# Kernel tuning notes

Hardware: AMD Instinct MI355X
Metric: run time of the kernel (lower is better)

Reference implementation:

```python
import jax, jax.numpy as jnp
import numpy as np
import math

D = 1024
H = 16
HD = D // H

def layernorm(x, g, b, eps=1e-5):
    mu = jnp.mean(x, axis=-1, keepdims=True)
    var = jnp.var(x, axis=-1, keepdims=True)
    return (x - mu) * jax.lax.rsqrt(var + eps) * g + b

def setup_inputs() -> dict:
    key = jax.random.key(0)
    ks = jax.random.split(key, 12)
    s = 0.02
    return {
        "x": jax.random.normal(ks[0], (2, 2048, D), jnp.float32),
        "Wk": jax.random.normal(ks[1], (D, D), jnp.float32) * s,
        "Wq": jax.random.normal(ks[2], (D, D), jnp.float32) * s,
        "Wv": jax.random.normal(ks[3], (D, D), jnp.float32) * s,
        "Wp": jax.random.normal(ks[4], (D, D), jnp.float32) * s,
        "bp": jnp.zeros((D,), jnp.float32),
        "g1": jnp.ones((D,), jnp.float32),
        "b1": jnp.zeros((D,), jnp.float32),
        "g2": jnp.ones((D,), jnp.float32),
        "b2": jnp.zeros((D,), jnp.float32),
        "W1": jax.random.normal(ks[5], (D, 4 * D), jnp.float32) * s,
        "bm1": jnp.zeros((4 * D,), jnp.float32),
        "W2": jax.random.normal(ks[6], (4 * D, D), jnp.float32) * s,
        "bm2": jnp.zeros((D,), jnp.float32),
    }

def reference(x, Wk, Wq, Wv, Wp, bp, g1, b1, g2, b2, W1, bm1, W2, bm2):
    B, S, _ = x.shape
    xn = layernorm(x, g1, b1)  # pre-LN; residual uses xn (faithful to source)
    # project and split heads -> [B, H, S, HD]
    def heads(y):
        return y.reshape(B, S, H, HD).transpose(0, 2, 1, 3)
    q = heads(xn @ Wq)
    k = heads(xn @ Wk)
    v = heads(xn @ Wv)
    scale = 1.0 / math.sqrt(HD)
    att = jnp.einsum('bhsd,bhtd->bhst', q, k) * scale  # [B,H,S,S]
    diag = jnp.eye(S, dtype=bool)
    att = jnp.where(diag, -jnp.inf, att)  # exclude self-attention on diagonal
    att = jax.nn.softmax(att, axis=-1)
    y = jnp.einsum('bhst,bhtd->bhsd', att, v)
    y = y.transpose(0, 2, 1, 3).reshape(B, S, D)
    y = y @ Wp + bp  # dropout is identity at inference
    h = xn + y
    hn = layernorm(h, g2, b2)
    mlp = jax.nn.gelu(hn @ W1 + bm1, approximate=False) @ W2 + bm2
    return h + mlp
```

## Files before the change

kernel.cpp:

```cpp
#include <hip/hip_runtime.h>
#include <hip/hip_bf16.h>
#include <math.h>

#define BATCH   2
#define SEQ     2048
#define D_MODEL 1024
#define NHEAD   16
#define HEADD   64
#define NROWS   (BATCH * SEQ)
#define D_FF    4096
#define TPARTS  4
#define TSPAN   (SEQ / TPARTS)

typedef __bf16 bf16_t;
typedef __bf16 bf16x2 __attribute__((ext_vector_type(2)));
typedef __bf16 bf16x4 __attribute__((ext_vector_type(4)));
typedef __bf16 bf16x8 __attribute__((ext_vector_type(8)));
typedef float  f32x4  __attribute__((ext_vector_type(4)));

#define QSCALE 0.18033688011112042f

__device__ __forceinline__ void gload_lds16(const void* g, void* l) {
    __builtin_amdgcn_global_load_lds(
        (const __attribute__((address_space(1))) unsigned int*)g,
        (__attribute__((address_space(3))) unsigned int*)l, 16, 0, 0);
}

__global__ __launch_bounds__(256) void transpose_all6(
    const float* __restrict__ Wq, const float* __restrict__ Wk,
    const float* __restrict__ Wv, const float* __restrict__ Wp,
    const float* __restrict__ W1, const float* __restrict__ W2,
    bf16_t* __restrict__ Wqkvt, bf16_t* __restrict__ Wpt,
    bf16_t* __restrict__ W1t, bf16_t* __restrict__ W2t)
{
    __shared__ float tile[32][33];
    int bid = blockIdx.x;
    const float* W; bf16_t* Wt; int K, N, n0, k0;
    if (bid < 4096) {
        int seg = bid >> 10, t = bid & 1023;
        W  = (seg == 0) ? Wq : (seg == 1) ? Wk : (seg == 2) ? Wv : Wp;
        Wt = (seg < 3) ? (Wqkvt + (size_t)seg * 1024 * 1024) : Wpt;
        K = 1024; N = 1024;
        n0 = (t & 31) * 32; k0 = (t >> 5) * 32;
    } else if (bid < 8192) {
        int t = bid - 4096;
        W = W1; Wt = W1t; K = 1024; N = 4096;
        n0 = (t & 127) * 32; k0 = (t >> 7) * 32;
    } else {
        int t = bid - 8192;
        W = W2; Wt = W2t; K = 4096; N = 1024;
        n0 = (t & 31) * 32; k0 = (t >> 5) * 32;
    }
    int tx = threadIdx.x;
    int ty = threadIdx.y;
    #pragma unroll
    for (int i = 0; i < 32; i += 8)
        tile[ty + i][tx] = W[(size_t)(k0 + ty + i) * N + n0 + tx];
    __syncthreads();
    #pragma unroll
    for (int i = 0; i < 32; i += 8)
        Wt[(size_t)(n0 + ty + i) * K + k0 + tx] = (bf16_t)tile[tx][ty + i];
}

__global__ __launch_bounds__(256) void ln_kernel(
    const float* __restrict__ x, const float* __restrict__ g,
    const float* __restrict__ b, bf16_t* __restrict__ out)
{
    int row = blockIdx.x;
    int tid = threadIdx.x;
    const float* xr = x + (size_t)row * D_MODEL;
    f32x4 v = *(const f32x4*)(xr + tid * 4);
    float s  = v[0] + v[1] + v[2] + v[3];
    float s2 = v[0]*v[0] + v[1]*v[1] + v[2]*v[2] + v[3]*v[3];
    #pragma unroll
    for (int off = 32; off; off >>= 1) {
        s  += __shfl_down(s, off);
        s2 += __shfl_down(s2, off);
    }
    __shared__ float ps[4], ps2[4];
    int w = tid >> 6, lane = tid & 63;
    if (lane == 0) { ps[w] = s; ps2[w] = s2; }
    __syncthreads();
    float sum  = ps[0] + ps[1] + ps[2] + ps[3];
    float sum2 = ps2[0] + ps2[1] + ps2[2] + ps2[3];
    float mu  = sum * (1.0f / D_MODEL);
    float var = sum2 * (1.0f / D_MODEL) - mu * mu;
    float rs  = rsqrtf(var + 1e-5f);
    #pragma unroll
    for (int j = 0; j < 4; ++j) {
        int c = tid * 4 + j;
        out[(size_t)row * D_MODEL + c] = (bf16_t)((v[j] - mu) * rs * g[c] + b[c]);
    }
}

__global__ __launch_bounds__(512) void gemm256_gelu(
    const bf16_t* __restrict__ A, const bf16_t* __restrict__ Bt,
    const float* __restrict__ bias, bf16_t* __restrict__ out,
    int M, int N, int K)
{
    __shared__ bf16_t As[2][256 * 64];
    __shared__ bf16_t Bs[2][256 * 64];
    int tid = threadIdx.x;
    int bid = blockIdx.x;
    int m0 = (bid & 15) * 256;
    int n0 = (bid >> 4) * 256;
    int w = tid >> 6, lane = tid & 63, quad = lane >> 4, l15 = lane & 15;
    int wm = (w >> 2) * 128;
    int wn = (w & 3) * 64;
    int rxs = l15 & 7;

    int srow = tid >> 3;
    int sxor = (((tid & 7) ^ (srow & 7)) << 3);
    const bf16_t* Ap = A  + (size_t)(m0 + srow) * K + sxor;
    const bf16_t* Bp = Bt + (size_t)(n0 + srow) * K + sxor;

    f32x4 acc[8][4] = {};

    int nt = K >> 6;
    {
        bf16_t* AsW = &As[0][w * 512];
        bf16_t* BsW = &Bs[0][w * 512];
        #pragma unroll
        for (int h = 0; h < 2; ++h)
            #pragma unroll
            for (int p = 0; p < 2; ++p) {
                gload_lds16(Ap + (size_t)(h * 128 + p * 64) * K, AsW + h * 8192 + p * 4096);
                gload_lds16(Bp + (size_t)(h * 128 + p * 64) * K, BsW + h * 8192 + p * 4096);
            }
    }

    for (int t = 0; t < nt; ++t) {
        int cur = t & 1;
        const bf16_t* Asc = &As[cur][0];
        const bf16_t* Bsc = &Bs[cur][0];
        bf16_t* AsN = &As[cur ^ 1][w * 512];
        bf16_t* BsN = &Bs[cur ^ 1][w * 512];
        bool pf = (t + 1 < nt);
        int k1 = (t + 1) << 6;
        asm volatile("s_waitcnt vmcnt(0)" ::: "memory");
        __builtin_amdgcn_s_barrier();
        __builtin_amdgcn_sched_barrier(0);

        bf16x8 bfr[4][2];
        #pragma unroll
        for (int q = 0; q < 4; ++q) {
            bf16x8 af[2][2];
            #pragma unroll
            for (int ii = 0; ii < 2; ++ii)
                #pragma unroll
                for (int kk = 0; kk < 2; ++kk)
                    af[ii][kk] = *(const bf16x8*)&Asc[(wm + (2 * q + ii) * 16 + l15) * 64
                                                      + (((kk * 4 + quad) ^ rxs) << 3)];
            if (q == 0) {
                #pragma unroll
                for (int j = 0; j < 4; ++j)
                    #pragma unroll
                    for (int kk = 0; kk < 2; ++kk)
                        bfr[j][kk] = *(const bf16x8*)&Bsc[(wn + j * 16 + l15) * 64
                                                          + (((kk * 4 + quad) ^ rxs) << 3)];
            }
            if (q == 0 && pf) {
                #pragma unroll
                for (int h = 0; h < 2; ++h)
                    #pragma unroll
                    for (int p = 0; p < 2; ++p)
                        gload_lds16(Ap + (size_t)(h * 128 + p * 64) * K + k1,
                                    AsN + h * 8192 + p * 4096);
            }
            if (q == 1 && pf) {
                #pragma unroll
                for (int h = 0; h < 2; ++h)
                    #pragma unroll
                    for (int p = 0; p < 2; ++p)
                        gload_lds16(Bp + (size_t)(h * 128 + p * 64) * K + k1,
                                    BsN + h * 8192 + p * 4096);
            }
            __builtin_amdgcn_s_barrier();
            asm volatile("s_waitcnt lgkmcnt(0)" ::: "memory");
            __builtin_amdgcn_sched_barrier(0);
            __builtin_amdgcn_s_setprio(1);
            #pragma unroll
            for (int ii = 0; ii < 2; ++ii)
                #pragma unroll
                for (int j = 0; j < 4; ++j)
                    #pragma unroll
                    for (int kk = 0; kk < 2; ++kk)
                        acc[2 * q + ii][j] = __builtin_amdgcn_mfma_f32_16x16x32_bf16(
                            af[ii][kk], bfr[j][kk], acc[2 * q + ii][j], 0, 0, 0);
            __builtin_amdgcn_s_setprio(0);
            __builtin_amdgcn_sched_barrier(0);
            __builtin_amdgcn_s_barrier();
        }
    }

    #pragma unroll
    for (int i = 0; i < 8; ++i)
    #pragma unroll
    for (int j = 0; j < 4; ++j) {
        int col  = n0 + wn + j * 16 + l15;
        int row0 = m0 + wm + i * 16 + quad * 4;
        float bv = bias[col];
        #pragma unroll
        for (int r = 0; r < 4; ++r) {
            int row = row0 + r;
            float u = acc[i][j][r] + bv;
            float y = u * (0.7978845608028654f + 0.03567740814f * u * u);
            float e = __builtin_amdgcn_exp2f(2.8853900817779268f * y);
            float r8 = __builtin_amdgcn_rcpf(e + 1.0f);
            out[(size_t)row * N + col] = (bf16_t)(u - u * r8);
        }
    }
}

template<int EPI, int BN>
__global__ __launch_bounds__(256) void gemm128(
    const bf16_t* __restrict__ A, const bf16_t* __restrict__ Bt,
    const float* __restrict__ bias, const void* __restrict__ resid,
    void* __restrict__ out, int M, int N, int K, int RY)
{
    constexpr int JN = BN / 32;
    constexpr int NBUF = (BN == 64) ? 3 : 2;
    __shared__ bf16_t As[NBUF][128 * 64];
    __shared__ bf16_t Bs[NBUF][BN * 64];
    int tid = threadIdx.x;
    int bid = blockIdx.x;
    int cx = bid & 3, cy = (bid >> 2) & 1, i0 = bid >> 3;
    int m0 = ((cx << 3) + (i0 & 7)) << 7;
    int n0 = (cy * RY + (i0 >> 3)) * BN;
    int w = tid >> 6, lane = tid & 63, quad = lane >> 4, l15 = lane & 15;
    int wm = (w & 1) * 64, wn = (w >> 1) * (BN / 2);
    int srow = tid >> 3;
    int sxor = (((tid & 7) ^ (srow & 7)) << 3);

    const bf16_t* Ap = A  + (size_t)(m0 + srow) * K + sxor;
    const bf16_t* Bp = Bt + (size_t)(n0 + srow) * K + sxor;

    int rxs = l15 & 7;

    auto stage = [&](int buf, int k0) {
        bf16_t* AsW = &As[buf][w * 512];
        bf16_t* BsW = &Bs[buf][w * 512];
        #pragma unroll
        for (int p = 0; p < 4; ++p)
            gload_lds16(Ap + (size_t)p * 32 * K + k0, AsW + p * 2048);
        #pragma unroll
        for (int p = 0; p < JN; ++p)
            gload_lds16(Bp + (size_t)p * 32 * K + k0, BsW + p * 2048);
    };

    f32x4 acc[4][JN] = {};

    int nt = K >> 6;
    stage(0, 0);
    if (NBUF == 3 && nt > 1) stage(1, 64);
    for (int t = 0; t < nt; ++t) {
        int cur = t % NBUF;
        if constexpr (NBUF == 3) {
            if (t + 2 < nt) {
                stage((t + 2) % NBUF, (t + 2) << 6);
                asm volatile("s_waitcnt vmcnt(12)" ::: "memory");
            } else if (t + 1 < nt) {
                asm volatile("s_waitcnt vmcnt(6)" ::: "memory");
            } else {
                asm volatile("s_waitcnt vmcnt(0)" ::: "memory");
            }
        } else {
            if (t + 1 < nt) {
                stage((t + 1) % NBUF, (t + 1) << 6);
                asm volatile("s_waitcnt vmcnt(8)" ::: "memory");
            } else {
                asm volatile("s_waitcnt vmcnt(0)" ::: "memory");
            }
        }
        __builtin_amdgcn_s_barrier();
        __builtin_amdgcn_sched_barrier(0);
        #pragma unroll
        for (int kk = 0; kk < 2; ++kk) {
            bf16x8 af[4], bfr[JN];
            #pragma unroll
            for (int i = 0; i < 4; ++i)
                af[i] = *(const bf16x8*)&As[cur][(wm + i * 16 + l15) * 64
                                            + ((((kk << 2) | quad) ^ rxs) << 3)];
            #pragma unroll
            for (int j = 0; j < JN; ++j)
                bfr[j] = *(const bf16x8*)&Bs[cur][(wn + j * 16 + l15) * 64
                                            + ((((kk << 2) | quad) ^ rxs) << 3)];
            #pragma unroll
            for (int i = 0; i < 4; ++i)
                #pragma unroll
                for (int j = 0; j < JN; ++j)
                    acc[i][j] = __builtin_amdgcn_mfma_f32_16x16x32_bf16(af[i], bfr[j], acc[i][j], 0, 0, 0);
        }
        __builtin_amdgcn_sched_barrier(0);
        asm volatile("s_waitcnt lgkmcnt(0)" ::: "memory");
        __builtin_amdgcn_s_barrier();
        __builtin_amdgcn_sched_barrier(0);
    }

    #pragma unroll
    for (int i = 0; i < 4; ++i)
    #pragma unroll
    for (int j = 0; j < JN; ++j) {
        int col  = n0 + wn + j * 16 + l15;
        int row0 = m0 + wm + i * 16 + quad * 4;
        if (EPI == 6) {
            int region = (n0 + wn + j * 16) >> 10;
            if (region < 2) {
                #pragma unroll
                for (int r = 0; r < 4; ++r) {
                    int row = row0 + r;
                    float v = acc[i][j][r];
                    if (region == 0) v *= QSCALE;
                    int b = row >> 11, s = row & 2047, hh = (col & 1023) >> 6, d = col & 63;
                    bf16_t* dst = (bf16_t*)out + (size_t)region * 4194304;
                    dst[(((size_t)(b * NHEAD + hh)) * SEQ + s) * HEADD + d] = (bf16_t)v;
                }
            } else {
                int dg = col - 2048, hh = dg >> 6, d = dg & 63;
                int b = row0 >> 11, s0 = row0 & 2047;
                bf16x4 pv;
                #pragma unroll
                for (int r = 0; r < 4; ++r) pv[r] = (bf16_t)acc[i][j][r];
                *(bf16x4*)((bf16_t*)out + 8388608
                           + (((size_t)(b * NHEAD + hh)) * HEADD + d) * SEQ + s0) = pv;
            }
        } else {
            float bv = bias[col];
            #pragma unroll
            for (int r = 0; r < 4; ++r) {
                int row = row0 + r;
                float vacc = acc[i][j][r] + bv;
                if (EPI == 1) {
                    float res = (float)((const bf16_t*)resid)[(size_t)row * N + col];
                    ((float*)out)[(size_t)row * N + col] = vacc + res;
                } else {
                    float res = ((const float*)resid)[(size_t)row * N + col];
                    ((float*)out)[(size_t)row * N + col] = vacc + res;
                }
            }
        }
    }
}

__global__ __launch_bounds__(256, 4) void attn_kernel(
    const bf16_t* __restrict__ q, const bf16_t* __restrict__ k,
    const bf16_t* __restrict__ vt, bf16_t* __restrict__ po,
    float* __restrict__ plsum)
{
    int gid = blockIdx.x;
    int xcd = gid & 7;
    int loc = gid >> 3;
    int bh  = xcd * 4 + (loc >> 6);
    int rest = loc & 63;
    int qt   = rest >> 2;
    int part = rest & 3;
    int tb0 = part * TSPAN, tend = tb0 + TSPAN;
    int b = bh >> 4, h = bh & 15;
    int tid = threadIdx.x, w = tid >> 6, lane = tid & 63;
    int quad = lane >> 4, l15 = lane & 15;
    int qbase = qt * 128 + w * 32;
    const bf16_t* qh = q  + (size_t)bh * SEQ * HEADD;
    const bf16_t* kh = k  + (size_t)bh * SEQ * HEADD;
    const bf16_t* vh = vt + (size_t)bh * HEADD * SEQ;

    bf16x8 qa[2][2];
    #pragma unroll
    for (int m = 0; m < 2; ++m)
        #pragma unroll
        for (int hf = 0; hf < 2; ++hf)
            qa[m][hf] = *(const bf16x8*)(qh + (size_t)(qbase + m * 16 + l15) * HEADD + hf * 32 + quad * 8);

    bf16x8 ones;
    #pragma unroll
    for (int j = 0; j < 8; ++j) ones[j] = (bf16_t)1.0f;

    __shared__ alignas(16) bf16_t Ks[32 * 72];
    __shared__ alignas(16) bf16_t Vs[64 * 40];
    __shared__ alignas(16) bf16_t Pl[4][32][40];

    int ksrow = tid >> 3, kscol = (tid & 7) * 8;
    int vsrow = tid >> 2, vscol = (tid & 3) * 8;
    const bf16_t* kg = kh + (size_t)ksrow * HEADD + kscol;
    const bf16_t* vg = vh + (size_t)vsrow * SEQ + vscol;

    f32x4 o[2][4] = {};
    f32x4 ls[2] = {};

    for (int t0 = tb0; t0 < tend; t0 += 32) {
        bf16x8 kreg = *(const bf16x8*)(kg + (size_t)t0 * HEADD);
        bf16x8 vreg = *(const bf16x8*)(vg + t0);
        __syncthreads();
        *(bf16x8*)&Ks[ksrow * 72 + kscol] = kreg;
        *(bf16x8*)&Vs[vsrow * 40 + vscol] = vreg;
        __syncthreads();

        bf16x8 kb[2][2], vf[4];
        #pragma unroll
        for (int jt = 0; jt < 2; ++jt)
            #pragma unroll
            for (int hf = 0; hf < 2; ++hf)
                kb[jt][hf] = *(const bf16x8*)&Ks[(2 * l15 + jt) * 72 + hf * 32 + quad * 8];
        #pragma unroll
        for (int dn = 0; dn < 4; ++dn)
            vf[dn] = *(const bf16x8*)&Vs[(dn * 16 + l15) * 40 + quad * 8];

        #pragma unroll
        for (int m = 0; m < 2; ++m) {
            f32x4 sc[2];
            #pragma unroll
            for (int jt = 0; jt < 2; ++jt) {
                f32x4 z = {};
                z = __builtin_amdgcn_mfma_f32_16x16x32_bf16(qa[m][0], kb[jt][0], z, 0, 0, 0);
                z = __builtin_amdgcn_mfma_f32_16x16x32_bf16(qa[m][1], kb[jt][1], z, 0, 0, 0);
                sc[jt] = z;
            }
            int qm = qbase + m * 16;
            bool dg = (t0 < qm + 16) && (t0 + 32 > qm);
            #pragma unroll
            for (int r = 0; r < 4; ++r) {
                int qrow = qm + quad * 4 + r;
                float p0 = __builtin_amdgcn_exp2f(sc[0][r]);
                float p1 = __builtin_amdgcn_exp2f(sc[1][r]);
                if (dg) {
                    int tg = t0 + 2 * l15;
                    if (tg == qrow)     p0 = 0.0f;
                    if (tg + 1 == qrow) p1 = 0.0f;
                }
                bf16x2 pp = { (bf16_t)p0, (bf16_t)p1 };
                *(bf16x2*)&Pl[w][m * 16 + quad * 4 + r][2 * l15] = pp;
            }
        }
        #pragma unroll
        for (int m = 0; m < 2; ++m) {
            bf16x8 pf = *(const bf16x8*)&Pl[w][m * 16 + l15][quad * 8];
            ls[m] = __builtin_amdgcn_mfma_f32_16x16x32_bf16(pf, ones, ls[m], 0, 0, 0);
            #pragma unroll
            for (int dn = 0; dn < 4; ++dn)
                o[m][dn] = __builtin_amdgcn_mfma_f32_16x16x32_bf16(pf, vf[dn], o[m][dn], 0, 0, 0);
        }
    }

    #pragma unroll
    for (int m = 0; m < 2; ++m)
        #pragma unroll
        for (int dn = 0; dn < 4; ++dn)
            #pragma unroll
            for (int r = 0; r < 4; ++r) {
                int qrow = qbase + m * 16 + quad * 4 + r;
                po[(((size_t)part * NROWS) + b * SEQ + qrow) * D_MODEL
                   + h * HEADD + dn * 16 + l15] = (bf16_t)o[m][dn][r];
            }
    if (l15 == 0) {
        #pragma unroll
        for (int m = 0; m < 2; ++m)
            #pragma unroll
            for (int r = 0; r < 4; ++r) {
                int qrow = qbase + m * 16 + quad * 4 + r;
                plsum[((size_t)part * 32 + bh) * SEQ + qrow] = ls[m][r];
            }
    }
}

__global__ __launch_bounds__(256) void attn_merge(
    const bf16_t* __restrict__ po, const float* __restrict__ plsum,
    bf16_t* __restrict__ y)
{
    int row = blockIdx.x;
    int tid = threadIdx.x;
    int c = tid * 4;
    int b = row >> 11, s = row & 2047;
    int bh = b * NHEAD + (c >> 6);
    float l = 0.0f;
    f32x4 ov = {};
    #pragma unroll
    for (int p = 0; p < TPARTS; ++p) {
        l += plsum[((size_t)p * 32 + bh) * SEQ + s];
        bf16x4 t = *(const bf16x4*)&po[((size_t)p * NROWS + row) * D_MODEL + c];
        #pragma unroll
        for (int j = 0; j < 4; ++j) ov[j] += (float)t[j];
    }
    float rl = 1.0f / l;
    bf16x4 out;
    #pragma unroll
    for (int j = 0; j < 4; ++j) out[j] = (bf16_t)(ov[j] * rl);
    *(bf16x4*)&y[(size_t)row * D_MODEL + c] = out;
}

extern "C" void kernel_launch(void* const* d_in, const int* in_sizes, int n_in,
                              void* d_out, int out_size, void* d_ws, size_t ws_size,
                              hipStream_t stream)
{
    const float* x   = (const float*)d_in[0];
    const float* Wk  = (const float*)d_in[1];
    const float* Wq  = (const float*)d_in[2];
    const float* Wv  = (const float*)d_in[3];
    const float* Wp  = (const float*)d_in[4];
    const float* bp  = (const float*)d_in[5];
    const float* g1  = (const float*)d_in[6];
    const float* b1  = (const float*)d_in[7];
    const float* g2  = (const float*)d_in[8];
    const float* b2  = (const float*)d_in[9];
    const float* W1  = (const float*)d_in[10];
    const float* bm1 = (const float*)d_in[11];
    const float* W2  = (const float*)d_in[12];
    const float* bm2 = (const float*)d_in[13];

    char* ws = (char*)d_ws;
    const size_t MB = 1024 * 1024;
    bf16_t* Wqkvt = (bf16_t*)(ws + 0 * MB);
    bf16_t* Wpt = (bf16_t*)(ws + 6 * MB);
    bf16_t* W1t = (bf16_t*)(ws + 8 * MB);
    bf16_t* W2t = (bf16_t*)(ws + 16 * MB);
    bf16_t* xn  = (bf16_t*)(ws + 24 * MB);
    bf16_t* qkv = (bf16_t*)(ws + 32 * MB);
    bf16_t* qb  = (bf16_t*)(ws + 32 * MB);
    bf16_t* kb  = (bf16_t*)(ws + 40 * MB);
    bf16_t* vtb = (bf16_t*)(ws + 48 * MB);
    bf16_t* yb  = (bf16_t*)(ws + 56 * MB);
    float*  hbuf= (float*) (ws + 64 * MB);
    bf16_t* po  = (bf16_t*)(ws + 64 * MB);
    float*  pls = (float*) (ws + 96 * MB);
    bf16_t* hn  = (bf16_t*)(ws + 24 * MB);
    bf16_t* act = (bf16_t*)(ws + 32 * MB);

    transpose_all6<<<12288, dim3(32, 8), 0, stream>>>(
        Wq, Wk, Wv, Wp, W1, W2, Wqkvt, Wpt, W1t, W2t);

    ln_kernel<<<NROWS, 256, 0, stream>>>(x, g1, b1, xn);

    gemm128<6, 128><<<768, 256, 0, stream>>>(xn, Wqkvt, nullptr, nullptr, qkv, NROWS, 3072, D_MODEL, 12);

    attn_kernel<<<2048, 256, 0, stream>>>(qb, kb, vtb, po, pls);
    attn_merge<<<NROWS, 256, 0, stream>>>(po, pls, yb);

    gemm128<1, 64><<<512, 256, 0, stream>>>(yb, Wpt, bp, xn, hbuf, NROWS, D_MODEL, D_MODEL, 8);

    ln_kernel<<<NROWS, 256, 0, stream>>>(hbuf, g2, b2, hn);

    gemm256_gelu<<<256, 512, 0, stream>>>(hn, W1t, bm1, act, NROWS, D_FF, D_MODEL);
    gemm128<3, 64><<<512, 256, 0, stream>>>(act, W2t, bm2, hbuf, d_out, NROWS, D_MODEL, D_FF, 8);
}
```

Measured before the change: 343.6 us.

## Restructure 256-tile GEMM pipeline with split LDS quarters and reuse it for QKV

The 256x256 GEMM is rewritten so each LDS buffer is split into four 64-row quarters. Prefetch of the next k-tile is staggered across four phases, with fine-grained vmcnt waits and fewer barriers per phase. The kernel is templated on the epilogue so the QKV projection (head-split scatter) also uses it, with 192 blocks of 512 threads replacing 768 blocks of 128x128 tiles. This aims to overlap global loads with MFMA work and raise reuse per tile, but the QKV grid of 192 blocks may under-fill the GPU's compute units.

```diff
diff --git a/kernel.cpp b/kernel.cpp
--- a/kernel.cpp
+++ b/kernel.cpp
@@ -93,103 +93,110 @@
     }
 }
 
-__global__ __launch_bounds__(512) void gemm256_gelu(
+template<int EPI>
+__global__ __launch_bounds__(512) void gemm256(
     const bf16_t* __restrict__ A, const bf16_t* __restrict__ Bt,
-    const float* __restrict__ bias, bf16_t* __restrict__ out,
+    const float* __restrict__ bias, void* __restrict__ out,
     int M, int N, int K)
 {
-    __shared__ bf16_t As[2][256 * 64];
-    __shared__ bf16_t Bs[2][256 * 64];
+    __shared__ bf16_t As[2][4][4096];
+    __shared__ bf16_t Bs[2][4][4096];
     int tid = threadIdx.x;
     int bid = blockIdx.x;
     int m0 = (bid & 15) * 256;
     int n0 = (bid >> 4) * 256;
     int w = tid >> 6, lane = tid & 63, quad = lane >> 4, l15 = lane & 15;
-    int wm = (w >> 2) * 128;
-    int wn = (w & 3) * 64;
+    int g = w >> 2;
+    int wm = g * 128, wn = (w & 3) * 64;
     int rxs = l15 & 7;
 
     int srow = tid >> 3;
-    int sxor = (((tid & 7) ^ (srow & 7)) << 3);
-    const bf16_t* Ap = A  + (size_t)(m0 + srow) * K + sxor;
-    const bf16_t* Bp = Bt + (size_t)(n0 + srow) * K + sxor;
+    int sx = (((tid & 7) ^ (srow & 7)) << 3);
+
+    const bf16_t* Asrc[4]; const bf16_t* Bsrc[4];
+    #pragma unroll
+    for (int r = 0; r < 4; ++r) {
+        int ra = (r & 1) * 128 + (r >> 1) * 64 + srow;
+        int rb = ((r & 1) * 2 + (srow >> 5)) * 64 + (r >> 1) * 32 + (srow & 31);
+        Asrc[r] = A  + (size_t)(m0 + ra) * K + sx;
+        Bsrc[r] = Bt + (size_t)(n0 + rb) * K + sx;
+    }
 
     f32x4 acc[8][4] = {};
-
     int nt = K >> 6;
-    {
-        bf16_t* AsW = &As[0][w * 512];
-        bf16_t* BsW = &Bs[0][w * 512];
-        #pragma unroll
-        for (int h = 0; h < 2; ++h)
-            #pragma unroll
-            for (int p = 0; p < 2; ++p) {
-                gload_lds16(Ap + (size_t)(h * 128 + p * 64) * K, AsW + h * 8192 + p * 4096);
-                gload_lds16(Bp + (size_t)(h * 128 + p * 64) * K, BsW + h * 8192 + p * 4096);
-            }
-    }
+
+    gload_lds16(Asrc[0], &As[0][0][w * 512]);
+    gload_lds16(Asrc[1], &As[0][1][w * 512]);
+    gload_lds16(Bsrc[0], &Bs[0][0][w * 512]);
+    gload_lds16(Bsrc[1], &Bs[0][1][w * 512]);
+    gload_lds16(Bsrc[2], &Bs[0][2][w * 512]);
+    gload_lds16(Bsrc[3], &Bs[0][3][w * 512]);
+    gload_lds16(Asrc[2], &As[0][2][w * 512]);
+    gload_lds16(Asrc[3], &As[0][3][w * 512]);
 
     for (int t = 0; t < nt; ++t) {
-        int cur = t & 1;
-        const bf16_t* Asc = &As[cur][0];
-        const bf16_t* Bsc = &Bs[cur][0];
-        bf16_t* AsN = &As[cur ^ 1][w * 512];
-        bf16_t* BsN = &Bs[cur ^ 1][w * 512];
+        int cur = t & 1, nb = cur ^ 1;
         bool pf = (t + 1 < nt);
         int k1 = (t + 1) << 6;
-        asm volatile("s_waitcnt vmcnt(0)" ::: "memory");
-        __builtin_amdgcn_s_barrier();
-        __builtin_amdgcn_sched_barrier(0);
-
-        bf16x8 bfr[4][2];
+        bf16x8 af[4][2];
         #pragma unroll
         for (int q = 0; q < 4; ++q) {
-            bf16x8 af[2][2];
-            #pragma unroll
-            for (int ii = 0; ii < 2; ++ii)
+            constexpr int dummy = 0; (void)dummy;
+            int ah = q >> 1, bh = q & 1;
+            if (q == 0) {
+                asm volatile("s_waitcnt vmcnt(4)" ::: "memory");
+            } else if (pf) {
+                if (q == 3) asm volatile("s_waitcnt vmcnt(6)" ::: "memory");
+                else        asm volatile("s_waitcnt vmcnt(4)" ::: "memory");
+            } else {
+                if (q == 1) asm volatile("s_waitcnt vmcnt(2)" ::: "memory");
+                else        asm volatile("s_waitcnt vmcnt(0)" ::: "memory");
+            }
+            __builtin_amdgcn_s_barrier();
+            __builtin_amdgcn_sched_barrier(0);
+            if (pf) {
+                if (q == 0) {
+                    gload_lds16(Asrc[0] + k1, &As[nb][0][w * 512]);
+                    gload_lds16(Asrc[1] + k1, &As[nb][1][w * 512]);
+                } else if (q == 1) {
+                    gload_lds16(Bsrc[0] + k1, &Bs[nb][0][w * 512]);
+                    gload_lds16(Bsrc[1] + k1, &Bs[nb][1][w * 512]);
+                } else if (q == 2) {
+                    gload_lds16(Bsrc[2] + k1, &Bs[nb][2][w * 512]);
+                    gload_lds16(Bsrc[3] + k1, &Bs[nb][3][w * 512]);
+                } else {
+                    gload_lds16(Asrc[2] + k1, &As[nb][2][w * 512]);
+                    gload_lds16(Asrc[3] + k1, &As[nb][3][w * 512]);
+                }
+            }
+            if ((q & 1) == 0) {
+                #pragma unroll
+                for (int ii = 0; ii < 4; ++ii)
+                    #pragma unroll
+                    for (int kk = 0; kk < 2; ++kk)
+                        af[ii][kk] = *(const bf16x8*)&As[cur][ah * 2 + g]
+                            [(ii * 16 + l15) * 64 + ((((kk << 2) | quad) ^ rxs) << 3)];
+            }
+            bf16x8 bfr[2][2];
+            #pragma unroll
+            for (int jj = 0; jj < 2; ++jj)
                 #pragma unroll
                 for (int kk = 0; kk < 2; ++kk)
-                    af[ii][kk] = *(const bf16x8*)&Asc[(wm + (2 * q + ii) * 16 + l15) * 64
-                                                      + (((kk * 4 + quad) ^ rxs) << 3)];
-            if (q == 0) {
-                #pragma unroll
-                for (int j = 0; j < 4; ++j)
-                    #pragma unroll
-                    for (int kk = 0; kk < 2; ++kk)
-                        bfr[j][kk] = *(const bf16x8*)&Bsc[(wn + j * 16 + l15) * 64
-                                                          + (((kk * 4 + quad) ^ rxs) << 3)];
-            }
-            if (q == 0 && pf) {
-                #pragma unroll
-                for (int h = 0; h < 2; ++h)
-                    #pragma unroll
-                    for (int p = 0; p < 2; ++p)
-                        gload_lds16(Ap + (size_t)(h * 128 + p * 64) * K + k1,
-                                    AsN + h * 8192 + p * 4096);
-            }
-            if (q == 1 && pf) {
-                #pragma unroll
-                for (int h = 0; h < 2; ++h)
-                    #pragma unroll
-                    for (int p = 0; p < 2; ++p)
-                        gload_lds16(Bp + (size_t)(h * 128 + p * 64) * K + k1,
-                                    BsN + h * 8192 + p * 4096);
-            }
-            __builtin_amdgcn_s_barrier();
+                    bfr[jj][kk] = *(const bf16x8*)&Bs[cur][bh * 2 + ((w >> 1) & 1)]
+                        [((w & 1) * 32 + jj * 16 + l15) * 64 + ((((kk << 2) | quad) ^ rxs) << 3)];
             asm volatile("s_waitcnt lgkmcnt(0)" ::: "memory");
             __builtin_amdgcn_sched_barrier(0);
             __builtin_amdgcn_s_setprio(1);
             #pragma unroll
-            for (int ii = 0; ii < 2; ++ii)
+            for (int ii = 0; ii < 4; ++ii)
                 #pragma unroll
-                for (int j = 0; j < 4; ++j)
+                for (int jj = 0; jj < 2; ++jj)
                     #pragma unroll
                     for (int kk = 0; kk < 2; ++kk)
-                        acc[2 * q + ii][j] = __builtin_amdgcn_mfma_f32_16x16x32_bf16(
-                            af[ii][kk], bfr[j][kk], acc[2 * q + ii][j], 0, 0, 0);
+                        acc[4 * ah + ii][2 * bh + jj] = __builtin_amdgcn_mfma_f32_16x16x32_bf16(
+                            af[ii][kk], bfr[jj][kk], acc[4 * ah + ii][2 * bh + jj], 0, 0, 0);
             __builtin_amdgcn_s_setprio(0);
             __builtin_amdgcn_sched_barrier(0);
-            __builtin_amdgcn_s_barrier();
         }
     }
 
@@ -197,110 +204,6 @@
     for (int i = 0; i < 8; ++i)
     #pragma unroll
     for (int j = 0; j < 4; ++j) {
-        int col  = n0 + wn + j * 16 + l15;
-        int row0 = m0 + wm + i * 16 + quad * 4;
-        float bv = bias[col];
-        #pragma unroll
-        for (int r = 0; r < 4; ++r) {
-            int row = row0 + r;
-            float u = acc[i][j][r] + bv;
-            float y = u * (0.7978845608028654f + 0.03567740814f * u * u);
-            float e = __builtin_amdgcn_exp2f(2.8853900817779268f * y);
-            float r8 = __builtin_amdgcn_rcpf(e + 1.0f);
-            out[(size_t)row * N + col] = (bf16_t)(u - u * r8);
-        }
-    }
-}
-
-template<int EPI, int BN>
-__global__ __launch_bounds__(256) void gemm128(
-    const bf16_t* __restrict__ A, const bf16_t* __restrict__ Bt,
-    const float* __restrict__ bias, const void* __restrict__ resid,
-    void* __restrict__ out, int M, int N, int K, int RY)
-{
-    constexpr int JN = BN / 32;
-    constexpr int NBUF = (BN == 64) ? 3 : 2;
-    __shared__ bf16_t As[NBUF][128 * 64];
-    __shared__ bf16_t Bs[NBUF][BN * 64];
-    int tid = threadIdx.x;
-    int bid = blockIdx.x;
-    int cx = bid & 3, cy = (bid >> 2) & 1, i0 = bid >> 3;
-    int m0 = ((cx << 3) + (i0 & 7)) << 7;
-    int n0 = (cy * RY + (i0 >> 3)) * BN;
-    int w = tid >> 6, lane = tid & 63, quad = lane >> 4, l15 = lane & 15;
-    int wm = (w & 1) * 64, wn = (w >> 1) * (BN / 2);
-    int srow = tid >> 3;
-    int sxor = (((tid & 7) ^ (srow & 7)) << 3);
-
-    const bf16_t* Ap = A  + (size_t)(m0 + srow) * K + sxor;
-    const bf16_t* Bp = Bt + (size_t)(n0 + srow) * K + sxor;
-
-    int rxs = l15 & 7;
-
-    auto stage = [&](int buf, int k0) {
-        bf16_t* AsW = &As[buf][w * 512];
-        bf16_t* BsW = &Bs[buf][w * 512];
-        #pragma unroll
-        for (int p = 0; p < 4; ++p)
-            gload_lds16(Ap + (size_t)p * 32 * K + k0, AsW + p * 2048);
-        #pragma unroll
-        for (int p = 0; p < JN; ++p)
-            gload_lds16(Bp + (size_t)p * 32 * K + k0, BsW + p * 2048);
-    };
-
-    f32x4 acc[4][JN] = {};
-
-    int nt = K >> 6;
-    stage(0, 0);
-    if (NBUF == 3 && nt > 1) stage(1, 64);
-    for (int t = 0; t < nt; ++t) {
-        int cur = t % NBUF;
-        if constexpr (NBUF == 3) {
-            if (t + 2 < nt) {
-                stage((t + 2) % NBUF, (t + 2) << 6);
-                asm volatile("s_waitcnt vmcnt(12)" ::: "memory");
-            } else if (t + 1 < nt) {
-                asm volatile("s_waitcnt vmcnt(6)" ::: "memory");
-            } else {
-                asm volatile("s_waitcnt vmcnt(0)" ::: "memory");
-            }
-        } else {
-            if (t + 1 < nt) {
-                stage((t + 1) % NBUF, (t + 1) << 6);
-                asm volatile("s_waitcnt vmcnt(8)" ::: "memory");
-            } else {
-                asm volatile("s_waitcnt vmcnt(0)" ::: "memory");
-            }
-        }
-        __builtin_amdgcn_s_barrier();
-        __builtin_amdgcn_sched_barrier(0);
-        #pragma unroll
-        for (int kk = 0; kk < 2; ++kk) {
-            bf16x8 af[4], bfr[JN];
-            #pragma unroll
-            for (int i = 0; i < 4; ++i)
-                af[i] = *(const bf16x8*)&As[cur][(wm + i * 16 + l15) * 64
-                                            + ((((kk << 2) | quad) ^ rxs) << 3)];
-            #pragma unroll
-            for (int j = 0; j < JN; ++j)
-                bfr[j] = *(const bf16x8*)&Bs[cur][(wn + j * 16 + l15) * 64
-                                            + ((((kk << 2) | quad) ^ rxs) << 3)];
-            #pragma unroll
-            for (int i = 0; i < 4; ++i)
-                #pragma unroll
-                for (int j = 0; j < JN; ++j)
-                    acc[i][j] = __builtin_amdgcn_mfma_f32_16x16x32_bf16(af[i], bfr[j], acc[i][j], 0, 0, 0);
-        }
-        __builtin_amdgcn_sched_barrier(0);
-        asm volatile("s_waitcnt lgkmcnt(0)" ::: "memory");
-        __builtin_amdgcn_s_barrier();
-        __builtin_amdgcn_sched_barrier(0);
-    }
-
-    #pragma unroll
-    for (int i = 0; i < 4; ++i)
-    #pragma unroll
-    for (int j = 0; j < JN; ++j) {
         int col  = n0 + wn + j * 16 + l15;
         int row0 = m0 + wm + i * 16 + quad * 4;
         if (EPI == 6) {
@@ -329,14 +232,118 @@
             #pragma unroll
             for (int r = 0; r < 4; ++r) {
                 int row = row0 + r;
-                float vacc = acc[i][j][r] + bv;
-                if (EPI == 1) {
-                    float res = (float)((const bf16_t*)resid)[(size_t)row * N + col];
-                    ((float*)out)[(size_t)row * N + col] = vacc + res;
-                } else {
-                    float res = ((const float*)resid)[(size_t)row * N + col];
-                    ((float*)out)[(size_t)row * N + col] = vacc + res;
-                }
+                float u = acc[i][j][r] + bv;
+                float y = u * (0.7978845608028654f + 0.03567740814f * u * u);
+                float e = __builtin_amdgcn_exp2f(2.8853900817779268f * y);
+                float r8 = __builtin_amdgcn_rcpf(e + 1.0f);
+                ((bf16_t*)out)[(size_t)row * N + col] = (bf16_t)(u - u * r8);
+            }
+        }
+    }
+}
+
+template<int EPI, int BN>
+__global__ __launch_bounds__(256) void gemm128(
+    const bf16_t* __restrict__ A, const bf16_t* __restrict__ Bt,
+    const float* __restrict__ bias, const void* __restrict__ resid,
+    void* __restrict__ out, int M, int N, int K, int RY)
+{
+    constexpr int JN = BN / 32;
+    constexpr int NBUF = (BN == 64) ? 3 : 2;
+    __shared__ bf16_t As[NBUF][128 * 64];
+    __shared__ bf16_t Bs[NBUF][BN * 64];
+    int tid = threadIdx.x;
+    int bid = blockIdx.x;
+    int cx = bid & 3, cy = (bid >> 2) & 1, i0 = bid >> 3;
+    int m0 = ((cx << 3) + (i0 & 7)) << 7;
+    int n0 = (cy * RY + (i0 >> 3)) * BN;
+    int w = tid >> 6, lane = tid & 63, quad = lane >> 4, l15 = lane & 15;
+    int wm = (w & 1) * 64, wn = (w >> 1) * (BN / 2);
+    int srow = tid >> 3;
+    int sxor = (((tid & 7) ^ (srow & 7)) << 3);
+
+    const bf16_t* Ap = A  + (size_t)(m0 + srow) * K + sxor;
+    const bf16_t* Bp = Bt + (size_t)(n0 + srow) * K + sxor;
+
+    int rxs = l15 & 7;
+
+    auto stage = [&](int buf, int k0) {
+        bf16_t* AsW = &As[buf][w * 512];
+        bf16_t* BsW = &Bs[buf][w * 512];
+        #pragma unroll
+        for (int p = 0; p < 4; ++p)
+            gload_lds16(Ap + (size_t)p * 32 * K + k0, AsW + p * 2048);
+        #pragma unroll
+        for (int p = 0; p < JN; ++p)
+            gload_lds16(Bp + (size_t)p * 32 * K + k0, BsW + p * 2048);
+    };
+
+    f32x4 acc[4][JN] = {};
+
+    int nt = K >> 6;
+    stage(0, 0);
+    if (NBUF == 3 && nt > 1) stage(1, 64);
+    for (int t = 0; t < nt; ++t) {
+        int cur = t % NBUF;
+        if constexpr (NBUF == 3) {
+            if (t + 2 < nt) {
+                stage((t + 2) % NBUF, (t + 2) << 6);
+                asm volatile("s_waitcnt vmcnt(12)" ::: "memory");
+            } else if (t + 1 < nt) {
+                asm volatile("s_waitcnt vmcnt(6)" ::: "memory");
+            } else {
+                asm volatile("s_waitcnt vmcnt(0)" ::: "memory");
+            }
+        } else {
+            if (t + 1 < nt) {
+                stage((t + 1) % NBUF, (t + 1) << 6);
+                asm volatile("s_waitcnt vmcnt(8)" ::: "memory");
+            } else {
+                asm volatile("s_waitcnt vmcnt(0)" ::: "memory");
+            }
+        }
+        __builtin_amdgcn_s_barrier();
+        __builtin_amdgcn_sched_barrier(0);
+        #pragma unroll
+        for (int kk = 0; kk < 2; ++kk) {
+            bf16x8 af[4], bfr[JN];
+            #pragma unroll
+            for (int i = 0; i < 4; ++i)
+                af[i] = *(const bf16x8*)&As[cur][(wm + i * 16 + l15) * 64
+                                            + ((((kk << 2) | quad) ^ rxs) << 3)];
+            #pragma unroll
+            for (int j = 0; j < JN; ++j)
+                bfr[j] = *(const bf16x8*)&Bs[cur][(wn + j * 16 + l15) * 64
+                                            + ((((kk << 2) | quad) ^ rxs) << 3)];
+            #pragma unroll
+            for (int i = 0; i < 4; ++i)
+                #pragma unroll
+                for (int j = 0; j < JN; ++j)
+                    acc[i][j] = __builtin_amdgcn_mfma_f32_16x16x32_bf16(af[i], bfr[j], acc[i][j], 0, 0, 0);
+        }
+        __builtin_amdgcn_sched_barrier(0);
+        asm volatile("s_waitcnt lgkmcnt(0)" ::: "memory");
+        __builtin_amdgcn_s_barrier();
+        __builtin_amdgcn_sched_barrier(0);
+    }
+
+    #pragma unroll
+    for (int i = 0; i < 4; ++i)
+    #pragma unroll
+    for (int j = 0; j < JN; ++j) {
+        int col  = n0 + wn + j * 16 + l15;
+        int row0 = m0 + wm + i * 16 + quad * 4;
+        float bv = bias[col];
+        #pragma unroll
+        for (int r = 0; r < 4; ++r) {
+            int row = row0 + r;
+            float vacc = acc[i][j][r] + bv;
+            if (EPI == 1) {
+                float res = (float)((const bf16_t*)resid)[(size_t)row * N + col];
+                ((float*)out)[(size_t)row * N + col] = vacc + res;
+            } else {
+                float res = ((const float*)resid)[(size_t)row * N + col];
+                ((float*)out)[(size_t)row * N + col] = vacc + res;
             }
         }
     }
@@ -528,7 +535,7 @@
 
     ln_kernel<<<NROWS, 256, 0, stream>>>(x, g1, b1, xn);
 
-    gemm128<6, 128><<<768, 256, 0, stream>>>(xn, Wqkvt, nullptr, nullptr, qkv, NROWS, 3072, D_MODEL, 12);
+    gemm256<6><<<192, 512, 0, stream>>>(xn, Wqkvt, nullptr, qkv, NROWS, 3072, D_MODEL);
 
     attn_kernel<<<2048, 256, 0, stream>>>(qb, kb, vtb, po, pls);
     attn_merge<<<NROWS, 256, 0, stream>>>(po, pls, yb);
@@ -537,6 +544,6 @@
 
     ln_kernel<<<NROWS, 256, 0, stream>>>(hbuf, g2, b2, hn);
 
-    gemm256_gelu<<<256, 512, 0, stream>>>(hn, W1t, bm1, act, NROWS, D_FF, D_MODEL);
+    gemm256<2><<<256, 512, 0, stream>>>(hn, W1t, bm1, act, NROWS, D_FF, D_MODEL);
     gemm128<3, 64><<<512, 256, 0, stream>>>(act, W2t, bm2, hbuf, d_out, NROWS, D_MODEL, D_FF, 8);
 }
```

Measured after the change: 370.1 us. 7.7% more time.
